# Kernel optimization log

Hardware: AMD Instinct MI355X
Metric: run time of the kernel (lower is better)

## Reference

```python
import jax, jax.numpy as jnp
import numpy as np

BS, N, HEADS, DIN, DOUT = 512, 128, 8, 64, 64


def setup_inputs() -> dict:
    key = jax.random.key(0)
    k1, k2, k3, k4, k5 = jax.random.split(key, 5)
    h = jax.random.normal(k1, (BS, N, DIN), dtype=jnp.float32)
    w = jax.random.normal(k2, (HEADS, DIN, DOUT), dtype=jnp.float32) * 0.1
    a_src = jax.random.normal(k3, (HEADS, DOUT, 1), dtype=jnp.float32) * 0.1
    a_dst = jax.random.normal(k4, (HEADS, DOUT, 1), dtype=jnp.float32) * 0.1
    bias = jnp.zeros((DOUT,), dtype=jnp.float32)
    # sparse random adjacency with self-loops so every softmax row is valid
    adj = jax.random.uniform(k5, (BS, N, N)) < 0.05
    adj = adj | jnp.eye(N, dtype=bool)[None, :, :]
    return {"h": h, "adj": adj, "w": w, "a_src": a_src, "a_dst": a_dst, "bias": bias}


def reference(h, adj, w, a_src, a_dst, bias):
    # h: [b, n, i]; w: [H, i, o] -> h_prime: [b, H, n, o]
    h_prime = jnp.einsum('bni,hio->bhno', h, w)
    t = jnp.tanh(h_prime)
    attn_src = jnp.einsum('bhno,ho->bhn', t, a_src[..., 0])  # [b, H, n]
    attn_dst = jnp.einsum('bhno,ho->bhn', t, a_dst[..., 0])  # [b, H, n]
    # attn[b,h,i,j] = src[b,h,i] + dst[b,h,j]
    attn = attn_src[..., :, None] + attn_dst[..., None, :]
    attn = jax.nn.leaky_relu(attn, negative_slope=0.2)
    attn = jnp.where(adj[:, None, :, :], attn, -jnp.inf)
    attn = jax.nn.softmax(attn, axis=-1)
    out = jnp.einsum('bhij,bhjo->bhio', attn, h_prime)
    return out + bias
```

## Files before the change

kernel.cpp:

```cpp
#include <hip/hip_runtime.h>

#define BSZ 512
#define NN 128
#define HEADS 8
#define DIN 64
#define DOUT 64

typedef __bf16 bf16x8 __attribute__((ext_vector_type(8)));
typedef float floatx4 __attribute__((ext_vector_type(4)));

static __device__ __forceinline__ unsigned short f2bf(float f) {
    __bf16 b = (__bf16)f;
    return __builtin_bit_cast(unsigned short, b);
}
static __device__ __forceinline__ bf16x8 ld_frag(const unsigned short* p) {
    uint4 r = *reinterpret_cast<const uint4*>(p);
    return __builtin_bit_cast(bf16x8, r);
}

__global__ __launch_bounds__(512) void pack_adj(
    const int* __restrict__ adj, unsigned int* __restrict__ msk)
{
    const int b = blockIdx.x;
    const int t = threadIdx.x;
    const int* ap = adj + (size_t)b * NN * NN + (t >> 2) * NN + (t & 3) * 32;
    unsigned int m = 0;
    #pragma unroll
    for (int q = 0; q < 8; ++q) {
        int4 v = *reinterpret_cast<const int4*>(ap + q * 4);
        m |= (v.x != 0 ? (1u << (4 * q + 0)) : 0u)
           | (v.y != 0 ? (1u << (4 * q + 1)) : 0u)
           | (v.z != 0 ? (1u << (4 * q + 2)) : 0u)
           | (v.w != 0 ? (1u << (4 * q + 3)) : 0u);
    }
    msk[b * 512 + t] = m;
}

__global__ __launch_bounds__(512, 6) void gat_fwd(
    const float* __restrict__ hin,
    const unsigned int* __restrict__ mskg,
    const float* __restrict__ w,
    const float* __restrict__ a_src,
    const float* __restrict__ a_dst,
    const float* __restrict__ bias,
    float* __restrict__ out)
{
    __shared__ __attribute__((aligned(16))) unsigned short hpT[DOUT * NN];
    __shared__ __attribute__((aligned(16))) unsigned short P[NN * NN];
    __shared__ __attribute__((aligned(16))) float s_src[NN];
    __shared__ __attribute__((aligned(16))) float s_dst[NN];

    const int bid  = blockIdx.x;
    const int b    = bid >> 3;
    const int hd   = bid & 7;
    const int tid  = threadIdx.x;
    const int lane = tid & 63;
    const int wv   = tid >> 6;
    const int lg   = lane >> 4;
    const int lm   = lane & 15;
    const int n0   = wv * 16;

    const float* hb = hin + (size_t)b * NN * DIN;
    bf16x8 hA[2];
    #pragma unroll
    for (int kt = 0; kt < 2; ++kt) {
        const float* p = hb + (n0 + lm) * DIN + kt * 32 + lg * 8;
        float4 v0 = *reinterpret_cast<const float4*>(p);
        float4 v1 = *reinterpret_cast<const float4*>(p + 4);
        bf16x8 a;
        a[0] = (__bf16)v0.x; a[1] = (__bf16)v0.y; a[2] = (__bf16)v0.z; a[3] = (__bf16)v0.w;
        a[4] = (__bf16)v1.x; a[5] = (__bf16)v1.y; a[6] = (__bf16)v1.z; a[7] = (__bf16)v1.w;
        hA[kt] = a;
    }
    const unsigned int mw = mskg[b * 512 + (n0 + lm) * 4 + lg];

    const float* wg = w + hd * DIN * DOUT;
    floatx4 acc[4] = {floatx4{0,0,0,0}, floatx4{0,0,0,0}, floatx4{0,0,0,0}, floatx4{0,0,0,0}};
    #pragma unroll
    for (int kt = 0; kt < 2; ++kt) {
        #pragma unroll
        for (int nt = 0; nt < 4; ++nt) {
            const float* wp = wg + (kt * 32 + lg * 8) * DOUT + nt * 16 + lm;
            bf16x8 bfr;
            #pragma unroll
            for (int q = 0; q < 8; ++q) bfr[q] = (__bf16)wp[q * DOUT];
            acc[nt] = __builtin_amdgcn_mfma_f32_16x16x32_bf16(hA[kt], bfr, acc[nt], 0, 0, 0);
        }
    }
    const float* asp = a_src + hd * DOUT;
    const float* adp = a_dst + hd * DOUT;
    float ps[4] = {0, 0, 0, 0}, pd[4] = {0, 0, 0, 0};
    #pragma unroll
    for (int nt = 0; nt < 4; ++nt) {
        const int o = nt * 16 + lm;
        const float as = asp[o], ad = adp[o];
        #pragma unroll
        for (int r = 0; r < 4; ++r) {
            const float v = acc[nt][r];
            const float ex = __expf(2.f * v);
            const float t = 1.f - 2.f / (ex + 1.f);
            ps[r] = fmaf(t, as, ps[r]);
            pd[r] = fmaf(t, ad, pd[r]);
        }
        const int jb = n0 + lg * 4;
        unsigned int u01 = f2bf(acc[nt][0]) | ((unsigned int)f2bf(acc[nt][1]) << 16);
        unsigned int u23 = f2bf(acc[nt][2]) | ((unsigned int)f2bf(acc[nt][3]) << 16);
        const int base = (o * 128 + jb) ^ ((o & 7) << 3);
        *reinterpret_cast<unsigned int*>(&hpT[base])     = u01;
        *reinterpret_cast<unsigned int*>(&hpT[base + 2]) = u23;
    }
    #pragma unroll
    for (int r = 0; r < 4; ++r) {
        #pragma unroll
        for (int m = 1; m <= 8; m <<= 1) {
            ps[r] += __shfl_xor(ps[r], m);
            pd[r] += __shfl_xor(pd[r], m);
        }
    }
    if (lm == 0) {
        #pragma unroll
        for (int r = 0; r < 4; ++r) {
            s_src[n0 + lg * 4 + r] = ps[r];
            s_dst[n0 + lg * 4 + r] = pd[r];
        }
    }
    __syncthreads();

    const int i = n0 + lm;
    const int sw = (i & 7) << 3;
    const float si = s_src[i];

    const int pz = i * 128 + lg * 32;
    #pragma unroll
    for (int t = 0; t < 4; ++t)
        *reinterpret_cast<uint4*>(&P[(pz + 8 * t) ^ sw]) = make_uint4(0, 0, 0, 0);

    unsigned int m = mw;
    float sum = 0.f;
    while (m) {
        const int q = __builtin_ctz(m); m &= m - 1;
        const float x = si + s_dst[lg * 32 + q];
        const float xl = fmaxf(x, 0.f) + 0.2f * fminf(x, 0.f);
        const float e = __expf(xl);
        const __bf16 eb = (__bf16)e;
        sum += (float)eb;
        P[(pz + q) ^ sw] = __builtin_bit_cast(unsigned short, eb);
    }
    sum += __shfl_xor(sum, 16);
    sum += __shfl_xor(sum, 32);
    const float inv = 1.f / sum;

    floatx4 oacc[4] = {floatx4{0,0,0,0}, floatx4{0,0,0,0}, floatx4{0,0,0,0}, floatx4{0,0,0,0}};
    #pragma unroll
    for (int kt = 0; kt < 4; ++kt) {
        const bf16x8 af = ld_frag(&P[(i * 128 + kt * 32 + lg * 8) ^ sw]);
        #pragma unroll
        for (int nt = 0; nt < 4; ++nt) {
            const int o = nt * 16 + lm;
            bf16x8 bfr = ld_frag(&hpT[(o * 128 + kt * 32 + lg * 8) ^ ((o & 7) << 3)]);
            oacc[nt] = __builtin_amdgcn_mfma_f32_16x16x32_bf16(af, bfr, oacc[nt], 0, 0, 0);
        }
    }
    float invr[4];
    #pragma unroll
    for (int r = 0; r < 4; ++r) invr[r] = __shfl(inv, lg * 4 + r);

    float* outb = out + ((size_t)b * HEADS + hd) * NN * DOUT;
    #pragma unroll
    for (int nt = 0; nt < 4; ++nt) {
        const int o = nt * 16 + lm;
        const float bo = bias[o];
        #pragma unroll
        for (int r = 0; r < 4; ++r) {
            const int row = n0 + lg * 4 + r;
            outb[row * DOUT + o] = fmaf(oacc[nt][r], invr[r], bo);
        }
    }
}

extern "C" void kernel_launch(void* const* d_in, const int* in_sizes, int n_in,
                              void* d_out, int out_size, void* d_ws, size_t ws_size,
                              hipStream_t stream) {
    (void)in_sizes; (void)n_in; (void)out_size; (void)ws_size;
    const float* h     = (const float*)d_in[0];
    const int*   adj   = (const int*)d_in[1];
    const float* w     = (const float*)d_in[2];
    const float* a_src = (const float*)d_in[3];
    const float* a_dst = (const float*)d_in[4];
    const float* bias  = (const float*)d_in[5];
    float* out = (float*)d_out;
    unsigned int* msk = (unsigned int*)d_ws;
    pack_adj<<<dim3(BSZ), dim3(512), 0, stream>>>(adj, msk);
    gat_fwd<<<dim3(BSZ * HEADS), dim3(512), 0, stream>>>(h, msk, w, a_src, a_dst, bias, out);
}
```

Baseline: 71.74 us.

## Pre-transpose weights to bf16 in prep kernel and vectorize output stores

The adjacency packing kernel now also converts W into a transposed bf16 layout in workspace, so each main-kernel block loads its weight fragments with single 16-byte loads. This replaces eight strided fp32 scalar loads plus conversions per fragment. The output MFMA swaps its operands so each lane holds four consecutive output columns of one row. Output is then written as float4 stores with vector bias loads, and the cross-lane shuffle of the normaliser is no longer needed. The weight path depends on workspace size, with a fallback to the old path.

```diff
diff --git a/kernel.cpp b/kernel.cpp
--- a/kernel.cpp
+++ b/kernel.cpp
@@ -18,8 +18,9 @@
     return __builtin_bit_cast(bf16x8, r);
 }
 
-__global__ __launch_bounds__(512) void pack_adj(
-    const int* __restrict__ adj, unsigned int* __restrict__ msk)
+__global__ __launch_bounds__(512) void prep(
+    const int* __restrict__ adj, const float* __restrict__ w,
+    unsigned int* __restrict__ msk, unsigned short* __restrict__ wT, int do_w)
 {
     const int b = blockIdx.x;
     const int t = threadIdx.x;
@@ -34,11 +35,26 @@
            | (v.w != 0 ? (1u << (4 * q + 3)) : 0u);
     }
     msk[b * 512 + t] = m;
+
+    if (do_w && b < HEADS) {
+        const float* wg = w + b * DIN * DOUT;
+        const int o = t >> 3, k0 = (t & 7) * 8;
+        unsigned int u[4];
+        #pragma unroll
+        for (int p = 0; p < 4; ++p) {
+            float f0 = wg[(k0 + 2 * p) * DOUT + o];
+            float f1 = wg[(k0 + 2 * p + 1) * DOUT + o];
+            u[p] = f2bf(f0) | ((unsigned int)f2bf(f1) << 16);
+        }
+        *reinterpret_cast<uint4*>(&wT[b * DOUT * DIN + o * DIN + k0]) =
+            make_uint4(u[0], u[1], u[2], u[3]);
+    }
 }
 
 __global__ __launch_bounds__(512, 6) void gat_fwd(
     const float* __restrict__ hin,
     const unsigned int* __restrict__ mskg,
+    const unsigned short* __restrict__ wTg,
     const float* __restrict__ w,
     const float* __restrict__ a_src,
     const float* __restrict__ a_dst,
@@ -74,17 +90,29 @@
     }
     const unsigned int mw = mskg[b * 512 + (n0 + lm) * 4 + lg];
 
-    const float* wg = w + hd * DIN * DOUT;
     floatx4 acc[4] = {floatx4{0,0,0,0}, floatx4{0,0,0,0}, floatx4{0,0,0,0}, floatx4{0,0,0,0}};
-    #pragma unroll
-    for (int kt = 0; kt < 2; ++kt) {
-        #pragma unroll
-        for (int nt = 0; nt < 4; ++nt) {
-            const float* wp = wg + (kt * 32 + lg * 8) * DOUT + nt * 16 + lm;
-            bf16x8 bfr;
+    if (wTg) {
+        const unsigned short* wt = wTg + hd * DOUT * DIN;
+        #pragma unroll
+        for (int kt = 0; kt < 2; ++kt) {
             #pragma unroll
-            for (int q = 0; q < 8; ++q) bfr[q] = (__bf16)wp[q * DOUT];
-            acc[nt] = __builtin_amdgcn_mfma_f32_16x16x32_bf16(hA[kt], bfr, acc[nt], 0, 0, 0);
+            for (int nt = 0; nt < 4; ++nt) {
+                bf16x8 bfr = ld_frag(&wt[(nt * 16 + lm) * DIN + kt * 32 + lg * 8]);
+                acc[nt] = __builtin_amdgcn_mfma_f32_16x16x32_bf16(hA[kt], bfr, acc[nt], 0, 0, 0);
+            }
+        }
+    } else {
+        const float* wg = w + hd * DIN * DOUT;
+        #pragma unroll
+        for (int kt = 0; kt < 2; ++kt) {
+            #pragma unroll
+            for (int nt = 0; nt < 4; ++nt) {
+                const float* wp = wg + (kt * 32 + lg * 8) * DOUT + nt * 16 + lm;
+                bf16x8 bfr;
+                #pragma unroll
+                for (int q = 0; q < 8; ++q) bfr[q] = (__bf16)wp[q * DOUT];
+                acc[nt] = __builtin_amdgcn_mfma_f32_16x16x32_bf16(hA[kt], bfr, acc[nt], 0, 0, 0);
+            }
         }
     }
     const float* asp = a_src + hd * DOUT;
@@ -158,30 +186,26 @@
         for (int nt = 0; nt < 4; ++nt) {
             const int o = nt * 16 + lm;
             bf16x8 bfr = ld_frag(&hpT[(o * 128 + kt * 32 + lg * 8) ^ ((o & 7) << 3)]);
-            oacc[nt] = __builtin_amdgcn_mfma_f32_16x16x32_bf16(af, bfr, oacc[nt], 0, 0, 0);
-        }
-    }
-    float invr[4];
-    #pragma unroll
-    for (int r = 0; r < 4; ++r) invr[r] = __shfl(inv, lg * 4 + r);
-
-    float* outb = out + ((size_t)b * HEADS + hd) * NN * DOUT;
+            oacc[nt] = __builtin_amdgcn_mfma_f32_16x16x32_bf16(bfr, af, oacc[nt], 0, 0, 0);
+        }
+    }
+    float* outr = out + (((size_t)b * HEADS + hd) * NN + (n0 + lm)) * DOUT;
     #pragma unroll
     for (int nt = 0; nt < 4; ++nt) {
-        const int o = nt * 16 + lm;
-        const float bo = bias[o];
-        #pragma unroll
-        for (int r = 0; r < 4; ++r) {
-            const int row = n0 + lg * 4 + r;
-            outb[row * DOUT + o] = fmaf(oacc[nt][r], invr[r], bo);
-        }
+        const float4 bv = *reinterpret_cast<const float4*>(&bias[nt * 16 + lg * 4]);
+        float4 st;
+        st.x = fmaf(oacc[nt][0], inv, bv.x);
+        st.y = fmaf(oacc[nt][1], inv, bv.y);
+        st.z = fmaf(oacc[nt][2], inv, bv.z);
+        st.w = fmaf(oacc[nt][3], inv, bv.w);
+        *reinterpret_cast<float4*>(&outr[nt * 16 + lg * 4]) = st;
     }
 }
 
 extern "C" void kernel_launch(void* const* d_in, const int* in_sizes, int n_in,
                               void* d_out, int out_size, void* d_ws, size_t ws_size,
                               hipStream_t stream) {
-    (void)in_sizes; (void)n_in; (void)out_size; (void)ws_size;
+    (void)in_sizes; (void)n_in; (void)out_size;
     const float* h     = (const float*)d_in[0];
     const int*   adj   = (const int*)d_in[1];
     const float* w     = (const float*)d_in[2];
@@ -189,7 +213,13 @@
     const float* a_dst = (const float*)d_in[4];
     const float* bias  = (const float*)d_in[5];
     float* out = (float*)d_out;
+
     unsigned int* msk = (unsigned int*)d_ws;
-    pack_adj<<<dim3(BSZ), dim3(512), 0, stream>>>(adj, msk);
-    gat_fwd<<<dim3(BSZ * HEADS), dim3(512), 0, stream>>>(h, msk, w, a_src, a_dst, bias, out);
-}
+    const size_t MSK_BYTES = (size_t)BSZ * 512 * 4;
+    unsigned short* wT = nullptr;
+    const bool use_wt = ws_size >= MSK_BYTES + (size_t)HEADS * DOUT * DIN * 2;
+    if (use_wt) wT = (unsigned short*)((char*)d_ws + MSK_BYTES);
+
+    prep<<<dim3(BSZ), dim3(512), 0, stream>>>(adj, w, msk, wT, use_wt ? 1 : 0);
+    gat_fwd<<<dim3(BSZ * HEADS), dim3(512), 0, stream>>>(h, msk, wT, w, a_src, a_dst, bias, out);
+}
```

After: 81.79 us. +14.0%, slower.
